# Kernel optimization log

Measured on AMD Instinct MI355X. Metric: run time of the kernel, lower is better.

Reference implementation:

```python
import jax, jax.numpy as jnp
import numpy as np
from jax import lax

V_, NC, SPW, H, B, T = 10000, 128, 64, 256, 16, 256  # C = NC*SPW = 8192
NEG = -1e9  # finite stand-in for -inf mask fill (grad-safe)


def _residual(x, w1, b1, w2, b2):
    # ResidualLayerOld: relu(lin2(relu(lin1(x)))) + x  (dropout=0 in eval)
    h = jax.nn.relu(x @ w1 + b1)
    return jax.nn.relu(h @ w2 + b2) + x


def _state_emb(e1, e2):
    # factored state embedding: state (c*SPW + j) -> e1[c] + e2[j]
    return (e1[:, None, :] + e2[None, :, :]).reshape(-1, e1.shape[-1])


def setup_inputs() -> dict:
    key = jax.random.key(0)
    ks = jax.random.split(key, 30)
    w2c = jax.random.randint(ks[0], (V_,), 0, NC)
    # brown-cluster style assignment: each word owns the SPW states of its cluster
    word2state = (w2c[:, None] * SPW + jnp.arange(SPW)[None, :]).astype(jnp.int32)
    text = jax.random.randint(ks[1], (B, T), 0, V_).astype(jnp.int32)

    def n(k, shape, s=0.05):
        return (jax.random.normal(k, shape) * s).astype(jnp.float32)

    z = lambda shape: jnp.zeros(shape, jnp.float32)
    return {
        "text": text, "word2state": word2state,
        "se1_start": n(ks[2], (NC, H), 1.0), "se2_start": n(ks[3], (SPW, H), 1.0),
        "start_w1": n(ks[4], (H, H)), "start_b1": z((H,)),
        "start_w2": n(ks[5], (H, H)), "start_b2": z((H,)),
        "start_pw": n(ks[6], (H, 1)), "start_pb": z((1,)),
        "se1_state": n(ks[7], (NC, H), 1.0), "se2_state": n(ks[8], (SPW, H), 1.0),
        "se1_next": n(ks[9], (NC, H), 1.0), "se2_next": n(ks[10], (SPW, H), 1.0),
        "trans_w1": n(ks[11], (H, H)), "trans_b1": z((H,)),
        "trans_w2": n(ks[12], (H, H)), "trans_b2": z((H,)),
        "se1_pre": n(ks[13], (NC, H), 1.0), "se2_pre": n(ks[14], (SPW, H), 1.0),
        "term_w1": n(ks[15], (H, H)), "term_b1": z((H,)),
        "term_w2": n(ks[16], (H, H)), "term_b2": z((H,)),
        "term_pw": n(ks[17], (H, V_)), "term_pb": z((V_,)),
    }


def reference(text, word2state,
              se1_start, se2_start, start_w1, start_b1, start_w2, start_b2,
              start_pw, start_pb,
              se1_state, se2_state, se1_next, se2_next,
              trans_w1, trans_b1, trans_w2, trans_b2,
              se1_pre, se2_pre, term_w1, term_b1, term_w2, term_b2,
              term_pw, term_pb):
    Vv, k = word2state.shape
    # start distribution over C states
    start_emb = _state_emb(se1_start, se2_start)                       # [C,H]
    start = jax.nn.log_softmax(
        (_residual(start_emb, start_w1, start_b1, start_w2, start_b2) @ start_pw
         + start_pb)[:, 0])                                            # [C]
    # transition: trans_mlp(state_emb) @ next_state_emb.T, row log_softmax
    state_emb = _state_emb(se1_state, se2_state)
    next_emb = _state_emb(se1_next, se2_next)
    transition = jax.nn.log_softmax(
        _residual(state_emb, trans_w1, trans_b1, trans_w2, trans_b2) @ next_emb.T,
        axis=-1)                                                       # [C,C]
    # emission: masked so state c only emits words whose word2state contains c
    pre_emb = _state_emb(se1_pre, se2_pre)
    C = pre_emb.shape[0]
    logits = _residual(pre_emb, term_w1, term_b1, term_w2, term_b2) @ term_pw + term_pb
    mask = jnp.zeros((C, Vv), dtype=bool).at[
        word2state.reshape(-1), jnp.repeat(jnp.arange(Vv), k)].set(True)
    emission = jax.nn.log_softmax(jnp.where(mask, logits, NEG), axis=-1)  # [C,V]
    # clamp to observed words
    cs = word2state[text]                                              # [B,T,k]
    pots = transition[cs[:, :-1, :, None], cs[:, 1:, None, :]]         # [B,T-1,k,k]
    obs = emission[cs, text[:, :, None]]                               # [B,T,k]
    alpha0 = start[cs[:, 0]] + obs[:, 0]                               # [B,k]

    def step(alpha, x):
        pot, o = x  # [B,k,k], [B,k]
        return jax.nn.logsumexp(alpha[:, :, None] + pot, axis=1) + o, None

    alpha, _ = lax.scan(step, alpha0,
                        (jnp.swapaxes(pots, 0, 1), jnp.swapaxes(obs[:, 1:], 0, 1)))
    return jax.nn.logsumexp(alpha, axis=-1)  # log p(text) per batch, [B]
```

## Files before the change

kernel.cpp:

```cpp
#include <hip/hip_runtime.h>
#include <hip/hip_bf16.h>
#include <math.h>

#define HH 256
#define NCC 128
#define SPWW 64
#define CST 8192
#define VV 10000
#define BBB 16
#define TTT 256
#define LOG2E 1.4426950408889634f
#define LN2 0.6931471805599453f

typedef __attribute__((ext_vector_type(8))) short short8;
typedef __attribute__((ext_vector_type(4))) float f32x4;
typedef unsigned short u16;

__device__ inline float bf2f(u16 u) {
    union { unsigned int i; float f; } v; v.i = ((unsigned int)u) << 16; return v.f;
}
__device__ inline u16 f2bf(float f) {
    __hip_bfloat16 h = __float2bfloat16(f);
    return *reinterpret_cast<u16*>(&h);
}
__device__ inline float ex2(float x) { return __builtin_amdgcn_exp2f(x); }
__device__ inline float lg2(float x) { return __builtin_amdgcn_logf(x); }

struct SetupA {
    const float* Ws[6]; u16* Wt;
    const float* pw; u16* pwT;
    const float* e1n; const float* e2n; u16* e1nb; u16* e2nb;
    const int* w2s; int* counts; int* offsets; int* wlist;
};
__global__ __launch_bounds__(256) void fhmm_setup(SetupA a)
{
    __shared__ float t[64][65];
    int blk = blockIdx.x, tid = threadIdx.x;
    if (blk < 96) {
        int z = blk >> 4, r = blk & 15;
        int k0 = (r & 3) * 64, n0 = (r >> 2) * 64;
        const float* W = a.Ws[z];
        u16* dst = a.Wt + (size_t)z * HH * HH;
        #pragma unroll
        for (int i = 0; i < 16; ++i) {
            int idx = tid + i * 256; int rr = idx >> 6, c = idx & 63;
            t[rr][c] = W[(k0 + rr) * HH + n0 + c];
        }
        __syncthreads();
        #pragma unroll
        for (int i = 0; i < 16; ++i) {
            int idx = tid + i * 256; int rr = idx >> 6, c = idx & 63;
            dst[(n0 + rr) * HH + k0 + c] = f2bf(t[c][rr]);
        }
    } else if (blk < 96 + 628) {
        int idx = blk - 96;
        int v0 = (idx % 157) * 64, k0 = (idx / 157) * 64;
        #pragma unroll
        for (int i = 0; i < 16; ++i) {
            int id2 = tid + i * 256; int rr = id2 >> 6, c = id2 & 63;
            int v = v0 + c;
            t[rr][c] = (v < VV) ? a.pw[(size_t)(k0 + rr) * VV + v] : 0.f;
        }
        __syncthreads();
        #pragma unroll
        for (int i = 0; i < 16; ++i) {
            int id2 = tid + i * 256; int rr = id2 >> 6, c = id2 & 63;
            int v = v0 + rr;
            if (v < VV) a.pwT[(size_t)v * HH + k0 + c] = f2bf(t[c][rr]);
        }
    } else if (blk < 96 + 628 + 128) {
        int idx = (blk - 724) * 256 + tid;
        if (idx < NCC * HH) a.e1nb[idx] = f2bf(a.e1n[idx]);
        if (idx < SPWW * HH) a.e2nb[idx] = f2bf(a.e2n[idx]);
    } else {
        __shared__ int cnt[NCC], off[NCC + 1], cur[NCC];
        if (tid < NCC) cnt[tid] = 0;
        __syncthreads();
        for (int v = tid; v < VV; v += 256)
            atomicAdd(&cnt[a.w2s[v * SPWW] >> 6], 1);
        __syncthreads();
        if (tid == 0) {
            int acc = 0;
            for (int c = 0; c < NCC; ++c) { off[c] = acc; acc += cnt[c]; }
            off[NCC] = acc;
        }
        __syncthreads();
        if (tid < NCC) cur[tid] = off[tid];
        __syncthreads();
        for (int v = tid; v < VV; v += 256) {
            int c = a.w2s[v * SPWW] >> 6;
            int pos = atomicAdd(&cur[c], 1);
            a.wlist[pos] = v;
        }
        if (tid < NCC) { a.counts[tid] = cnt[tid]; a.offsets[tid] = off[tid]; }
        if (tid == 0) a.offsets[NCC] = off[NCC];
    }
}

struct MlpA {
    const u16* X[3];
    const float* se1[3]; const float* se2[3];
    const u16* Wth[3];
    const float* bias[3];
    u16* Y[3];
    float oscale[3];
};
template<int LAYER>
__global__ __launch_bounds__(256) void fhmm_mlp_batch(MlpA a)
{
    int hd = blockIdx.z;
    int m0 = blockIdx.x * 64, n0 = blockIdx.y * 64;
    __shared__ char Xs[32768];
    __shared__ char Ws[32768];
    int tid = threadIdx.x, w = tid >> 6, lane = tid & 63, lr = lane & 15, lg = lane >> 4;
    const char* wsrc = (const char*)(a.Wth[hd] + (size_t)n0 * HH);
    if (LAYER == 0) {
        const float* s1 = a.se1[hd];
        const float* s2 = a.se2[hd];
        #pragma unroll
        for (int i = 0; i < 8; ++i) {
            int cc = i * 256 + tid; int row = cc >> 5, tt = cc & 31;
            int gm = m0 + row, k = tt * 8;
            const float* p1 = s1 + (gm >> 6) * HH + k;
            const float* p2 = s2 + (gm & 63) * HH + k;
            u16 pk[8];
            #pragma unroll
            for (int e = 0; e < 8; ++e) pk[e] = f2bf(p1[e] + p2[e]);
            int dst = row * 512 + ((tt ^ (row & 7)) << 4);
            *(uint4*)&Xs[dst] = *(uint4*)pk;
            *(uint4*)&Ws[dst] = *(const uint4*)(wsrc + cc * 16);
        }
    } else {
        const char* xsrc = (const char*)(a.X[hd] + (size_t)m0 * HH);
        #pragma unroll
        for (int i = 0; i < 8; ++i) {
            int cc = i * 256 + tid; int row = cc >> 5, tt = cc & 31;
            int dst = row * 512 + ((tt ^ (row & 7)) << 4);
            *(uint4*)&Xs[dst] = *(const uint4*)(xsrc + cc * 16);
            *(uint4*)&Ws[dst] = *(const uint4*)(wsrc + cc * 16);
        }
    }
    __syncthreads();
    short8 bfr[8];
    int brow = w * 16 + lr, bb = brow * 512, bsw = (brow & 7) << 4;
    #pragma unroll
    for (int ks = 0; ks < 8; ++ks)
        bfr[ks] = *(const short8*)(Ws + bb + (((ks * 4 + lg) << 4) ^ bsw));
    int cb = w * 16 + lg * 4;
    f32x4 bv = *(const f32x4*)(a.bias[hd] + n0 + cb);
    float osc = a.oscale[hd];
    u16* Yp = a.Y[hd];
    #pragma unroll
    for (int rm = 0; rm < 4; ++rm) {
        f32x4 acc = {0.f, 0.f, 0.f, 0.f};
        int ar = rm * 16 + lr, ab = ar * 512, asw = (ar & 7) << 4;
        #pragma unroll
        for (int ks = 0; ks < 8; ++ks) {
            short8 af = *(const short8*)(Xs + ab + (((ks * 4 + lg) << 4) ^ asw));
            acc = __builtin_amdgcn_mfma_f32_16x16x32_bf16(bfr[ks], af, acc, 0, 0, 0);
        }
        int gm = m0 + rm * 16 + lr;
        ushort4 o;
        if (LAYER == 1) {
            const float* r1 = a.se1[hd] + (gm >> 6) * HH + n0 + cb;
            const float* r2 = a.se2[hd] + (gm & 63) * HH + n0 + cb;
            #pragma unroll
            for (int e = 0; e < 4; ++e)
                ((u16*)&o)[e] = f2bf((fmaxf(acc[e] + bv[e], 0.f) + r1[e] + r2[e]) * osc);
        } else {
            #pragma unroll
            for (int e = 0; e < 4; ++e)
                ((u16*)&o)[e] = f2bf(fmaxf(acc[e] + bv[e], 0.f));
        }
        *(ushort4*)(Yp + (size_t)gm * HH + n0 + cb) = o;
    }
}

__global__ __launch_bounds__(256) void fhmm_gemm_uv(
    const u16* __restrict__ Abf, const u16* __restrict__ e1n,
    const u16* __restrict__ e2n, float* __restrict__ U2, float* __restrict__ V2)
{
    int y = blockIdx.y;
    int m0 = blockIdx.x * 64;
    const u16* Bb; float* C; int ldc;
    if (y < 2) { Bb = e1n + (size_t)y * 64 * HH; C = U2 + y * 64; ldc = NCC; }
    else       { Bb = e2n;                        C = V2;          ldc = SPWW; }
    __shared__ char Xs[32768];
    __shared__ char Ws[32768];
    int tid = threadIdx.x, w = tid >> 6, lane = tid & 63, lr = lane & 15, lg = lane >> 4;
    const char* xsrc = (const char*)(Abf + (size_t)m0 * HH);
    const char* wsrc = (const char*)Bb;
    #pragma unroll
    for (int i = 0; i < 8; ++i) {
        int cc = i * 256 + tid; int row = cc >> 5, tt = cc & 31;
        int dst = row * 512 + ((tt ^ (row & 7)) << 4);
        *(uint4*)&Xs[dst] = *(const uint4*)(xsrc + cc * 16);
        *(uint4*)&Ws[dst] = *(const uint4*)(wsrc + cc * 16);
    }
    __syncthreads();
    short8 bfr[8];
    int brow = w * 16 + lr, bb = brow * 512, bsw = (brow & 7) << 4;
    #pragma unroll
    for (int ks = 0; ks < 8; ++ks)
        bfr[ks] = *(const short8*)(Ws + bb + (((ks * 4 + lg) << 4) ^ bsw));
    int cb = w * 16 + lg * 4;
    #pragma unroll
    for (int rm = 0; rm < 4; ++rm) {
        f32x4 acc = {0.f, 0.f, 0.f, 0.f};
        int ar = rm * 16 + lr, ab = ar * 512, asw = (ar & 7) << 4;
        #pragma unroll
        for (int ks = 0; ks < 8; ++ks) {
            short8 af = *(const short8*)(Xs + ab + (((ks * 4 + lg) << 4) ^ asw));
            acc = __builtin_amdgcn_mfma_f32_16x16x32_bf16(bfr[ks], af, acc, 0, 0, 0);
        }
        int gm = m0 + rm * 16 + lr;
        *(f32x4*)(C + (size_t)gm * ldc + cb) = acc;
    }
}

__global__ __launch_bounds__(256) void fhmm_lse_uv(
    const float* __restrict__ U2, const float* __restrict__ V2,
    float* __restrict__ lse2)
{
    int tid = threadIdx.x, w = tid >> 6, lane = tid & 63;
    int s = blockIdx.x * 4 + w;
    float u0 = U2[(size_t)s * NCC + lane];
    float u1 = U2[(size_t)s * NCC + 64 + lane];
    float vv = V2[(size_t)s * SPWW + lane];
    float mu = fmaxf(u0, u1);
    #pragma unroll
    for (int d = 32; d; d >>= 1) mu = fmaxf(mu, __shfl_xor(mu, d));
    float su = ex2(u0 - mu) + ex2(u1 - mu);
    #pragma unroll
    for (int d = 32; d; d >>= 1) su += __shfl_xor(su, d);
    float mv = vv;
    #pragma unroll
    for (int d = 32; d; d >>= 1) mv = fmaxf(mv, __shfl_xor(mv, d));
    float sv = ex2(vv - mv);
    #pragma unroll
    for (int d = 32; d; d >>= 1) sv += __shfl_xor(sv, d);
    if (lane == 0) lse2[s] = (mu + lg2(su)) + (mv + lg2(sv));
}

__global__ __launch_bounds__(256) void fhmm_dotpw_kernel(
    const u16* __restrict__ hb, const float* __restrict__ pw,
    const float* __restrict__ pbp, float* __restrict__ p)
{
    int wv = threadIdx.x >> 6;
    int lane = threadIdx.x & 63;
    int s = blockIdx.x * 4 + wv;
    const u16* hr = hb + (size_t)s * HH;
    float acc = 0.f;
    #pragma unroll
    for (int i = 0; i < 4; ++i) acc += bf2f(hr[i * 64 + lane]) * pw[i * 64 + lane];
    #pragma unroll
    for (int d = 32; d; d >>= 1) acc += __shfl_xor(acc, d);
    if (lane == 0) p[s] = acc + pbp[0];
}

__global__ __launch_bounds__(1024) void fhmm_lsm_vec_kernel(float* __restrict__ p)
{
    __shared__ float red[64];
    int tid = threadIdx.x;
    float m = -1e30f;
    for (int i = tid; i < CST; i += 1024) m = fmaxf(m, p[i]);
    #pragma unroll
    for (int d = 32; d; d >>= 1) m = fmaxf(m, __shfl_xor(m, d));
    if ((tid & 63) == 0) red[tid >> 6] = m;
    __syncthreads();
    if (tid == 0) {
        float mm = red[0];
        for (int q = 1; q < 16; ++q) mm = fmaxf(mm, red[q]);
        red[32] = mm;
    }
    __syncthreads();
    float M = red[32];
    float s = 0.f;
    for (int i = tid; i < CST; i += 1024) s += expf(p[i] - M);
    #pragma unroll
    for (int d = 32; d; d >>= 1) s += __shfl_xor(s, d);
    if ((tid & 63) == 0) red[tid >> 6] = s;
    __syncthreads();
    if (tid == 0) {
        float ss = 0.f;
        for (int q = 0; q < 16; ++q) ss += red[q];
        red[33] = ss;
    }
    __syncthreads();
    float lse = M + logf(red[33]);
    for (int i = tid; i < CST; i += 1024) p[i] -= lse;
}

__global__ __launch_bounds__(256) void fhmm_ew_mfma(
    const u16* __restrict__ hpre_bf, const u16* __restrict__ pwT,
    const float* __restrict__ pb, const int* __restrict__ wlist,
    const int* __restrict__ counts, const int* __restrict__ offsets,
    float* __restrict__ Ew2, float* __restrict__ lse_em2)
{
    int c = blockIdx.x;
    int cnt = counts[c], off = offsets[c];
    __shared__ char Hs[32768];
    __shared__ float emM[4][64], emS[4][64];
    int tid = threadIdx.x, w = tid >> 6, lane = tid & 63, lr = lane & 15, lg = lane >> 4;
    const char* src = (const char*)(hpre_bf + (size_t)c * 64 * HH);
    #pragma unroll
    for (int i = 0; i < 8; ++i) {
        int cc = i * 256 + tid; int row = cc >> 5, tt = cc & 31;
        *(uint4*)&Hs[row * 512 + ((tt ^ (row & 7)) << 4)] = *(const uint4*)(src + cc * 16);
    }
    __syncthreads();

    float em_m[4][4], em_s[4][4];
    #pragma unroll
    for (int rm = 0; rm < 4; ++rm)
        #pragma unroll
        for (int e = 0; e < 4; ++e) { em_m[rm][e] = -3e38f; em_s[rm][e] = 0.f; }

    for (int ch = 0; ch * 64 < cnt; ++ch) {
        int widx = ch * 64 + w * 16 + lr;
        bool valid = widx < cnt;
        int v = valid ? wlist[off + widx] : 0;
        short8 bw[8];
        short8 bz = {0, 0, 0, 0, 0, 0, 0, 0};
        #pragma unroll
        for (int ks = 0; ks < 8; ++ks)
            bw[ks] = valid ? *(const short8*)(pwT + (size_t)v * HH + ks * 32 + lg * 8) : bz;
        float pbv = valid ? pb[v] : 0.f;
        #pragma unroll
        for (int rm = 0; rm < 4; ++rm) {
            f32x4 acc = {0.f, 0.f, 0.f, 0.f};
            int ar = rm * 16 + lr, ab = ar * 512, asw = (ar & 7) << 4;
            #pragma unroll
            for (int ks = 0; ks < 8; ++ks) {
                short8 ah = *(const short8*)(Hs + ab + (((ks * 4 + lg) << 4) ^ asw));
                acc = __builtin_amdgcn_mfma_f32_16x16x32_bf16(ah, bw[ks], acc, 0, 0, 0);
            }
            f32x4 o;
            #pragma unroll
            for (int e = 0; e < 4; ++e) o[e] = (acc[e] + pbv) * LOG2E;
            if (valid)
                *(f32x4*)(Ew2 + (size_t)v * 64 + rm * 16 + lg * 4) = o;
            #pragma unroll
            for (int e = 0; e < 4; ++e) {
                if (valid) {
                    float mn = fmaxf(em_m[rm][e], o[e]);
                    em_s[rm][e] = em_s[rm][e] * ex2(em_m[rm][e] - mn) + ex2(o[e] - mn);
                    em_m[rm][e] = mn;
                }
            }
        }
    }

    #pragma unroll
    for (int rm = 0; rm < 4; ++rm)
        #pragma unroll
        for (int e = 0; e < 4; ++e) {
            float mm = em_m[rm][e], ss = em_s[rm][e];
            #pragma unroll
            for (int d = 1; d < 16; d <<= 1) {
                float m2 = __shfl_xor(mm, d);
                float s2 = __shfl_xor(ss, d);
                float mn = fmaxf(mm, m2);
                ss = ss * ex2(mm - mn) + s2 * ex2(m2 - mn);
                mm = mn;
            }
            em_m[rm][e] = mm; em_s[rm][e] = ss;
        }
    if (lr == 0) {
        #pragma unroll
        for (int rm = 0; rm < 4; ++rm)
            #pragma unroll
            for (int e = 0; e < 4; ++e) {
                emM[w][rm * 16 + lg * 4 + e] = em_m[rm][e];
                emS[w][rm * 16 + lg * 4 + e] = em_s[rm][e];
            }
    }
    __syncthreads();
    if (tid < 64) {
        float M = emM[0][tid], S = emS[0][tid];
        #pragma unroll
        for (int q2 = 1; q2 < 4; ++q2) {
            float m2 = emM[q2][tid], s2 = emS[q2][tid];
            float mn = fmaxf(M, m2);
            S = S * ex2(M - mn) + s2 * ex2(m2 - mn); M = mn;
        }
        lse_em2[c * 64 + tid] = M + lg2(fmaxf(S, 1e-33f));
    }
}

template<int LEAF>
__global__ __launch_bounds__(256) void fhmm_combine4(
    const float* __restrict__ U2, const float* __restrict__ V2,
    const float* __restrict__ Ew2, const float* __restrict__ lse_em2,
    const float* __restrict__ lse2,
    const int* __restrict__ text, const int* __restrict__ w2s,
    const float* __restrict__ Lin, float* __restrict__ Lout)
{
    int p = blockIdx.x, b = blockIdx.y;
    int nodes = gridDim.x;
    int tid = threadIdx.x;
    int l6 = tid & 63, q = tid >> 6;

    __shared__ float Rb[64][65];
    __shared__ char Ps[8192], Qs[8192];
    __shared__ float mA2[64], mB2[64], mAf[64], mBf[64];
    __shared__ float part[2][4][64];
    __shared__ float rtB_l[64];

    int nm = LEAF ? ((p == 63) ? 3 : 4) : 4;
    int t0 = 4 * p + 1;
    int in0 = 4 * p;

    float va[16];
    float rowA = 0.f;

    if (LEAF) {
        int vprev = text[b * TTT + (t0 - 1)];
        int vA = text[b * TTT + t0];
        int srA = w2s[vprev * SPWW];
        int sA = w2s[vA * SPWW];
        int cA = sA >> 6;
        rowA = U2[(size_t)(srA + l6) * NCC + cA] - lse2[srA + l6];
        const float* vrow = V2 + (size_t)(srA + l6) * SPWW;
        const float* ewA = Ew2 + (size_t)vA * 64;
        const float* leA = lse_em2 + sA;
        #pragma unroll
        for (int jj = 0; jj < 16; ++jj) {
            int j = q * 16 + jj;
            va[jj] = vrow[j] + ewA[j] - leA[j];
        }
    } else {
        const float* Af = Lin + ((size_t)(b * (4 * nodes) + in0)) * 4096;
        #pragma unroll
        for (int jj = 0; jj < 16; ++jj)
            va[jj] = Af[l6 * 64 + q * 16 + jj];
    }

    for (int s = 1; s < nm; ++s) {
        float mloc = -3e38f;
        #pragma unroll
        for (int jj = 0; jj < 16; ++jj) mloc = fmaxf(mloc, va[jj]);
        part[0][q][l6] = mloc;

        float vb[16], obB = 0.f;
        if (LEAF) {
            int tB = t0 + s;
            int vBp = text[b * TTT + (tB - 1)];
            int vB = text[b * TTT + tB];
            int srB = w2s[vBp * SPWW];
            int sB = w2s[vB * SPWW];
            int cB = sB >> 6;
            if (tid < 64)
                rtB_l[tid] = U2[(size_t)(srB + tid) * NCC + cB] - lse2[srB + tid];
            obB = Ew2[(size_t)vB * 64 + l6] - lse_em2[sB + l6];
            float vraw[16];
            #pragma unroll
            for (int kk = 0; kk < 16; ++kk)
                vraw[kk] = V2[(size_t)(srB + q * 16 + kk) * SPWW + l6];
            __syncthreads();
            float mlocB = -3e38f;
            #pragma unroll
            for (int kk = 0; kk < 16; ++kk) {
                vb[kk] = vraw[kk] + rtB_l[q * 16 + kk];
                mlocB = fmaxf(mlocB, vb[kk]);
            }
            part[1][q][l6] = mlocB;
        } else {
            const float* Bf = Lin + ((size_t)(b * (4 * nodes) + in0 + s)) * 4096;
            float mlocB = -3e38f;
            #pragma unroll
            for (int kk = 0; kk < 16; ++kk) {
                float v = Bf[(q * 16 + kk) * 64 + l6];
                vb[kk] = v; mlocB = fmaxf(mlocB, v);
            }
            part[1][q][l6] = mlocB;
        }
        __syncthreads();

        if (tid < 64) {
            float mf = fmaxf(fmaxf(part[0][0][tid], part[0][1][tid]),
                             fmaxf(part[0][2][tid], part[0][3][tid]));
            mAf[tid] = mf;
            mA2[tid] = mf + ((LEAF && s == 1) ? rowA : 0.f);
        } else if (tid < 128) {
            int j = tid & 63;
            float mf = fmaxf(fmaxf(part[1][0][j], part[1][1][j]),
                             fmaxf(part[1][2][j], part[1][3][j]));
            mBf[j] = mf;
            mB2[j] = mf + obB;
        }
        __syncthreads();

        {
            float ma = mAf[l6];
            u16 pk[16];
            #pragma unroll
            for (int e = 0; e < 16; ++e) pk[e] = f2bf(ex2(va[e] - ma));
            uint4* srcv = (uint4*)pk;
            int base = l6 * 128;
            int s0 = 2 * q, s1 = 2 * q + 1, sw = (l6 & 7);
            *(uint4*)&Ps[base + ((s0 ^ sw) << 4)] = srcv[0];
            *(uint4*)&Ps[base + ((s1 ^ sw) << 4)] = srcv[1];
            float mb = mBf[l6];
            #pragma unroll
            for (int e = 0; e < 16; ++e) pk[e] = f2bf(ex2(vb[e] - mb));
            *(uint4*)&Qs[base + ((s0 ^ sw) << 4)] = srcv[0];
            *(uint4*)&Qs[base + ((s1 ^ sw) << 4)] = srcv[1];
        }
        __syncthreads();

        int w = q, lr = l6 & 15, lg = l6 >> 4;
        int brow = w * 16 + lr;
        short8 bfr[2];
        #pragma unroll
        for (int ks = 0; ks < 2; ++ks)
            bfr[ks] = *(const short8*)(Qs + brow * 128 + (((ks * 4 + lg) << 4) ^ ((brow & 7) << 4)));
        bool last = (s == nm - 1);
        float* Co = Lout + ((size_t)(b * nodes + p)) * 4096;
        #pragma unroll
        for (int rm = 0; rm < 4; ++rm) {
            f32x4 acc = {0.f, 0.f, 0.f, 0.f};
            int ar = rm * 16 + lr;
            #pragma unroll
            for (int ks = 0; ks < 2; ++ks) {
                short8 af = *(const short8*)(Ps + ar * 128 + (((ks * 4 + lg) << 4) ^ ((ar & 7) << 4)));
                acc = __builtin_amdgcn_mfma_f32_16x16x32_bf16(af, bfr[ks], acc, 0, 0, 0);
            }
            #pragma unroll
            for (int e = 0; e < 4; ++e) {
                int ii = rm * 16 + lg * 4 + e;
                int jj = w * 16 + lr;
                float cv = mA2[ii] + mB2[jj] + lg2(fmaxf(acc[e], 1e-33f));
                if (last) Co[ii * 64 + jj] = cv;
                else      Rb[ii][jj] = cv;
            }
        }
        if (!last) {
            __syncthreads();
            #pragma unroll
            for (int jj = 0; jj < 16; ++jj)
                va[jj] = Rb[l6][q * 16 + jj];
        }
    }
}

__global__ __launch_bounds__(256) void fhmm_tree_final(
    const float* __restrict__ Lin,
    const float* __restrict__ startv, const float* __restrict__ Ew2,
    const float* __restrict__ lse_em2,
    const int* __restrict__ text, const int* __restrict__ w2s,
    float* __restrict__ out)
{
    int b = blockIdx.x;
    int tid = threadIdx.x;
    int l6 = tid & 63, q = tid >> 6;

    __shared__ float Rb[64][65];
    __shared__ char Ps[8192], Qs[8192];
    __shared__ float mA2[64], mB2[64], mAf[64], mBf[64];
    __shared__ float part[2][4][64];
    __shared__ float a0[64];
    __shared__ float rm_[4], rs_[4];

    float va[16];
    {
        const float* Af = Lin + ((size_t)(b * 4)) * 4096;
        #pragma unroll
        for (int jj = 0; jj < 16; ++jj)
            va[jj] = Af[l6 * 64 + q * 16 + jj];
    }

    for (int s = 1; s < 4; ++s) {
        float mloc = -3e38f;
        #pragma unroll
        for (int jj = 0; jj < 16; ++jj) mloc = fmaxf(mloc, va[jj]);
        part[0][q][l6] = mloc;

        const float* Bf = Lin + ((size_t)(b * 4 + s)) * 4096;
        float vb[16];
        float mlocB = -3e38f;
        #pragma unroll
        for (int kk = 0; kk < 16; ++kk) {
            float v = Bf[(q * 16 + kk) * 64 + l6];
            vb[kk] = v; mlocB = fmaxf(mlocB, v);
        }
        part[1][q][l6] = mlocB;
        __syncthreads();

        if (tid < 64) {
            float mf = fmaxf(fmaxf(part[0][0][tid], part[0][1][tid]),
                             fmaxf(part[0][2][tid], part[0][3][tid]));
            mAf[tid] = mf; mA2[tid] = mf;
        } else if (tid < 128) {
            int j = tid & 63;
            float mf = fmaxf(fmaxf(part[1][0][j], part[1][1][j]),
                             fmaxf(part[1][2][j], part[1][3][j]));
            mBf[j] = mf; mB2[j] = mf;
        }
        __syncthreads();

        {
            float ma = mAf[l6];
            u16 pk[16];
            #pragma unroll
            for (int e = 0; e < 16; ++e) pk[e] = f2bf(ex2(va[e] - ma));
            uint4* srcv = (uint4*)pk;
            int base = l6 * 128;
            int s0 = 2 * q, s1 = 2 * q + 1, sw = (l6 & 7);
            *(uint4*)&Ps[base + ((s0 ^ sw) << 4)] = srcv[0];
            *(uint4*)&Ps[base + ((s1 ^ sw) << 4)] = srcv[1];
            float mb = mBf[l6];
            #pragma unroll
            for (int e = 0; e < 16; ++e) pk[e] = f2bf(ex2(vb[e] - mb));
            *(uint4*)&Qs[base + ((s0 ^ sw) << 4)] = srcv[0];
            *(uint4*)&Qs[base + ((s1 ^ sw) << 4)] = srcv[1];
        }
        __syncthreads();

        int w = q, lr = l6 & 15, lg = l6 >> 4;
        int brow = w * 16 + lr;
        short8 bfr[2];
        #pragma unroll
        for (int ks = 0; ks < 2; ++ks)
            bfr[ks] = *(const short8*)(Qs + brow * 128 + (((ks * 4 + lg) << 4) ^ ((brow & 7) << 4)));
        #pragma unroll
        for (int rm = 0; rm < 4; ++rm) {
            f32x4 acc = {0.f, 0.f, 0.f, 0.f};
            int ar = rm * 16 + lr;
            #pragma unroll
            for (int ks = 0; ks < 2; ++ks) {
                short8 af = *(const short8*)(Ps + ar * 128 + (((ks * 4 + lg) << 4) ^ ((ar & 7) << 4)));
                acc = __builtin_amdgcn_mfma_f32_16x16x32_bf16(af, bfr[ks], acc, 0, 0, 0);
            }
            #pragma unroll
            for (int e = 0; e < 4; ++e) {
                int ii = rm * 16 + lg * 4 + e;
                int jj = w * 16 + lr;
                Rb[ii][jj] = mA2[ii] + mB2[jj] + lg2(fmaxf(acc[e], 1e-33f));
            }
        }
        __syncthreads();
        if (s < 3) {
            #pragma unroll
            for (int jj = 0; jj < 16; ++jj)
                va[jj] = Rb[l6][q * 16 + jj];
        }
    }

    if (tid < 64) {
        int v0 = text[b * TTT];
        int s0 = w2s[v0 * SPWW];
        a0[tid] = startv[s0 + tid] * LOG2E + Ew2[(size_t)v0 * 64 + tid] - lse_em2[s0 + tid];
    }
    __syncthreads();
    float m = -3e38f, s = 0.f;
    for (int e = tid; e < 4096; e += 256) {
        float v = a0[e >> 6] + Rb[e >> 6][e & 63];
        float mn = fmaxf(m, v);
        s = s * ex2(m - mn) + ex2(v - mn);
        m = mn;
    }
    #pragma unroll
    for (int d = 32; d; d >>= 1) {
        float m2 = __shfl_xor(m, d), sx = __shfl_xor(s, d);
        float mn = fmaxf(m, m2);
        s = s * ex2(m - mn) + sx * ex2(m2 - mn); m = mn;
    }
    if ((tid & 63) == 0) { rm_[tid >> 6] = m; rs_[tid >> 6] = s; }
    __syncthreads();
    if (tid == 0) {
        float M_ = rm_[0], S_ = rs_[0];
        #pragma unroll
        for (int qq = 1; qq < 4; ++qq) {
            float mn = fmaxf(M_, rm_[qq]);
            S_ = S_ * ex2(M_ - mn) + rs_[qq] * ex2(rm_[qq] - mn); M_ = mn;
        }
        out[b] = (M_ + lg2(S_)) * LN2;
    }
}

extern "C" void kernel_launch(void* const* d_in, const int* in_sizes, int n_in,
                              void* d_out, int out_size, void* d_ws, size_t ws_size,
                              hipStream_t stream) {
    const int* text        = (const int*)d_in[0];
    const int* w2s         = (const int*)d_in[1];
    const float* se1_start = (const float*)d_in[2];
    const float* se2_start = (const float*)d_in[3];
    const float* start_w1  = (const float*)d_in[4];
    const float* start_b1  = (const float*)d_in[5];
    const float* start_w2  = (const float*)d_in[6];
    const float* start_b2  = (const float*)d_in[7];
    const float* start_pw  = (const float*)d_in[8];
    const float* start_pb  = (const float*)d_in[9];
    const float* se1_state = (const float*)d_in[10];
    const float* se2_state = (const float*)d_in[11];
    const float* se1_next  = (const float*)d_in[12];
    const float* se2_next  = (const float*)d_in[13];
    const float* trans_w1  = (const float*)d_in[14];
    const float* trans_b1  = (const float*)d_in[15];
    const float* trans_w2  = (const float*)d_in[16];
    const float* trans_b2  = (const float*)d_in[17];
    const float* se1_pre   = (const float*)d_in[18];
    const float* se2_pre   = (const float*)d_in[19];
    const float* term_w1   = (const float*)d_in[20];
    const float* term_b1   = (const float*)d_in[21];
    const float* term_w2   = (const float*)d_in[22];
    const float* term_b2   = (const float*)d_in[23];
    const float* term_pw   = (const float*)d_in[24];
    const float* term_pb   = (const float*)d_in[25];
    float* out = (float*)d_out;

    char* wp = (char*)d_ws;
    auto alloc = [&](size_t bytes) {
        char* p = wp;
        wp += (bytes + 255) & ~(size_t)255;
        return (void*)p;
    };
    u16* h1a         = (u16*)alloc((size_t)CST * HH * 2);
    u16* h1b         = (u16*)alloc((size_t)CST * HH * 2);
    u16* h1c         = (u16*)alloc((size_t)CST * HH * 2);
    u16* hstart_bf   = (u16*)alloc((size_t)CST * HH * 2);
    u16* h_state_bf  = (u16*)alloc((size_t)CST * HH * 2);
    u16* h_pre_bf    = (u16*)alloc((size_t)CST * HH * 2);
    u16* Wt          = (u16*)alloc((size_t)6 * HH * HH * 2);
    u16* pwT         = (u16*)alloc((size_t)VV * HH * 2);
    u16* e1n_bf      = (u16*)alloc((size_t)NCC * HH * 2);
    u16* e2n_bf      = (u16*)alloc((size_t)SPWW * HH * 2);
    float* U2        = (float*)alloc((size_t)CST * NCC * 4);
    float* V2        = (float*)alloc((size_t)CST * SPWW * 4);
    float* startv    = (float*)alloc(CST * 4);
    float* lse_trans = (float*)alloc(CST * 4);
    float* lse_em    = (float*)alloc(CST * 4);
    float* Ew        = (float*)alloc((size_t)VV * 64 * 4);
    int* counts      = (int*)alloc(NCC * 4);
    int* offsets     = (int*)alloc((NCC + 4) * 4);
    int* wlist       = (int*)alloc(VV * 4);
    float* LvA       = (float*)alloc((size_t)BBB * 64 * 4096 * 4);
    float* LvB       = (float*)alloc((size_t)BBB * 16 * 4096 * 4);
    float* LvC       = (float*)alloc((size_t)BBB * 4 * 4096 * 4);

    SetupA sa;
    sa.Ws[0] = start_w1; sa.Ws[1] = start_w2; sa.Ws[2] = trans_w1;
    sa.Ws[3] = trans_w2; sa.Ws[4] = term_w1;  sa.Ws[5] = term_w2;
    sa.Wt = Wt; sa.pw = term_pw; sa.pwT = pwT;
    sa.e1n = se1_next; sa.e2n = se2_next; sa.e1nb = e1n_bf; sa.e2nb = e2n_bf;
    sa.w2s = w2s; sa.counts = counts; sa.offsets = offsets; sa.wlist = wlist;
    hipLaunchKernelGGL(fhmm_setup, dim3(853), 256, 0, stream, sa);

    MlpA m1;
    m1.X[0] = m1.X[1] = m1.X[2] = nullptr;
    m1.se1[0] = se1_start; m1.se1[1] = se1_state; m1.se1[2] = se1_pre;
    m1.se2[0] = se2_start; m1.se2[1] = se2_state; m1.se2[2] = se2_pre;
    m1.Wth[0] = Wt + 0 * HH * HH; m1.Wth[1] = Wt + 2 * HH * HH; m1.Wth[2] = Wt + 4 * HH * HH;
    m1.bias[0] = start_b1; m1.bias[1] = trans_b1; m1.bias[2] = term_b1;
    m1.Y[0] = h1a; m1.Y[1] = h1b; m1.Y[2] = h1c;
    m1.oscale[0] = m1.oscale[1] = m1.oscale[2] = 1.0f;
    hipLaunchKernelGGL((fhmm_mlp_batch<0>), dim3(128, 4, 3), 256, 0, stream, m1);

    MlpA m2 = m1;
    m2.X[0] = h1a; m2.X[1] = h1b; m2.X[2] = h1c;
    m2.Wth[0] = Wt + 1 * HH * HH; m2.Wth[1] = Wt + 3 * HH * HH; m2.Wth[2] = Wt + 5 * HH * HH;
    m2.bias[0] = start_b2; m2.bias[1] = trans_b2; m2.bias[2] = term_b2;
    m2.Y[0] = hstart_bf; m2.Y[1] = h_state_bf; m2.Y[2] = h_pre_bf;
    m2.oscale[0] = 1.0f; m2.oscale[1] = LOG2E; m2.oscale[2] = 1.0f;
    hipLaunchKernelGGL((fhmm_mlp_batch<1>), dim3(128, 4, 3), 256, 0, stream, m2);

    hipLaunchKernelGGL(fhmm_dotpw_kernel, dim3(2048), 256, 0, stream,
                       hstart_bf, start_pw, start_pb, startv);
    hipLaunchKernelGGL(fhmm_lsm_vec_kernel, dim3(1), 1024, 0, stream, startv);

    hipLaunchKernelGGL(fhmm_gemm_uv, dim3(128, 3), 256, 0, stream,
                       h_state_bf, e1n_bf, e2n_bf, U2, V2);
    hipLaunchKernelGGL(fhmm_lse_uv, dim3(2048), 256, 0, stream, U2, V2, lse_trans);

    hipLaunchKernelGGL(fhmm_ew_mfma, dim3(NCC), 256, 0, stream,
                       h_pre_bf, pwT, term_pb, wlist, counts, offsets, Ew, lse_em);

    hipLaunchKernelGGL((fhmm_combine4<1>), dim3(64, BBB), 256, 0, stream,
                       U2, V2, Ew, lse_em, lse_trans, text, w2s,
                       (const float*)nullptr, LvA);
    hipLaunchKernelGGL((fhmm_combine4<0>), dim3(16, BBB), 256, 0, stream,
                       (const float*)nullptr, (const float*)nullptr,
                       (const float*)nullptr, (const float*)nullptr,
                       (const float*)nullptr, (const int*)nullptr,
                       (const int*)nullptr, LvA, LvB);
    hipLaunchKernelGGL((fhmm_combine4<0>), dim3(4, BBB), 256, 0, stream,
                       (const float*)nullptr, (const float*)nullptr,
                       (const float*)nullptr, (const float*)nullptr,
                       (const float*)nullptr, (const int*)nullptr,
                       (const int*)nullptr, LvB, LvC);

    hipLaunchKernelGGL(fhmm_tree_final, dim3(BBB), 256, 0, stream,
                       LvC, startv, Ew, lse_em, text, w2s, out);
}
```

Before: 125.6 us.

## Fuse start projection, UV log-sum-exp and start normalization into neighbouring kernels

The start head's final dot product with start_pw now runs in the second MLP layer's epilogue, using shuffles and atomicAdd into a zeroed startv buffer. This drops the separate dot kernel and the write of hstart_bf. The start log-softmax kernel is removed: its log-sum-exp is computed inside the combine kernel and subtracted from the final output, which is valid because start enters the likelihood once as an additive shift. The U/V GEMM and its row log-sum-exp are merged into one kernel that loops over the three weight tiles with online max/sum, trading 384 blocks for 128 and fewer launches and re-reads of U2/V2.

After: 126.5 us. Within noise of the previous version (+0.7%).

```diff
diff --git a/kernel.cpp b/kernel.cpp
--- a/kernel.cpp
+++ b/kernel.cpp
@@ -31,6 +31,7 @@
     const float* pw; u16* pwT;
     const float* e1n; const float* e2n; u16* e1nb; u16* e2nb;
     const int* w2s; int* counts; int* offsets; int* wlist;
+    float* startv;
 };
 __global__ __launch_bounds__(256) void fhmm_setup(SetupA a)
 {
@@ -52,7 +53,7 @@
             int idx = tid + i * 256; int rr = idx >> 6, c = idx & 63;
             dst[(n0 + rr) * HH + k0 + c] = f2bf(t[c][rr]);
         }
-    } else if (blk < 96 + 628) {
+    } else if (blk < 724) {
         int idx = blk - 96;
         int v0 = (idx % 157) * 64, k0 = (idx / 157) * 64;
         #pragma unroll
@@ -68,10 +69,13 @@
             int v = v0 + rr;
             if (v < VV) a.pwT[(size_t)v * HH + k0 + c] = f2bf(t[c][rr]);
         }
-    } else if (blk < 96 + 628 + 128) {
+    } else if (blk < 852) {
         int idx = (blk - 724) * 256 + tid;
         if (idx < NCC * HH) a.e1nb[idx] = f2bf(a.e1n[idx]);
         if (idx < SPWW * HH) a.e2nb[idx] = f2bf(a.e2n[idx]);
+    } else if (blk < 884) {
+        int idx = (blk - 852) * 256 + tid;
+        if (idx < CST) a.startv[idx] = 0.f;
     } else {
         __shared__ int cnt[NCC], off[NCC + 1], cur[NCC];
         if (tid < NCC) cnt[tid] = 0;
@@ -104,6 +108,8 @@
     const float* bias[3];
     u16* Y[3];
     float oscale[3];
+    const float* pw;
+    float* startv;
 };
 template<int LAYER>
 __global__ __launch_bounds__(256) void fhmm_mlp_batch(MlpA a)
@@ -160,135 +166,139 @@
             acc = __builtin_amdgcn_mfma_f32_16x16x32_bf16(bfr[ks], af, acc, 0, 0, 0);
         }
         int gm = m0 + rm * 16 + lr;
-        ushort4 o;
         if (LAYER == 1) {
             const float* r1 = a.se1[hd] + (gm >> 6) * HH + n0 + cb;
             const float* r2 = a.se2[hd] + (gm & 63) * HH + n0 + cb;
+            float vals[4];
             #pragma unroll
             for (int e = 0; e < 4; ++e)
-                ((u16*)&o)[e] = f2bf((fmaxf(acc[e] + bv[e], 0.f) + r1[e] + r2[e]) * osc);
+                vals[e] = fmaxf(acc[e] + bv[e], 0.f) + r1[e] + r2[e];
+            if (hd == 0) {
+                const float* pwc = a.pw + n0 + cb;
+                float dotp = vals[0] * pwc[0] + vals[1] * pwc[1]
+                           + vals[2] * pwc[2] + vals[3] * pwc[3];
+                dotp += __shfl_xor(dotp, 16);
+                dotp += __shfl_xor(dotp, 32);
+                if (lg == 0) atomicAdd(&a.startv[gm], dotp);
+            } else {
+                ushort4 o;
+                #pragma unroll
+                for (int e = 0; e < 4; ++e) ((u16*)&o)[e] = f2bf(vals[e] * osc);
+                *(ushort4*)(Yp + (size_t)gm * HH + n0 + cb) = o;
+            }
         } else {
+            ushort4 o;
             #pragma unroll
             for (int e = 0; e < 4; ++e)
                 ((u16*)&o)[e] = f2bf(fmaxf(acc[e] + bv[e], 0.f));
-        }
-        *(ushort4*)(Yp + (size_t)gm * HH + n0 + cb) = o;
+            *(ushort4*)(Yp + (size_t)gm * HH + n0 + cb) = o;
+        }
     }
 }
 
-__global__ __launch_bounds__(256) void fhmm_gemm_uv(
+__global__ __launch_bounds__(256) void fhmm_gemm_uv_lse(
     const u16* __restrict__ Abf, const u16* __restrict__ e1n,
-    const u16* __restrict__ e2n, float* __restrict__ U2, float* __restrict__ V2)
+    const u16* __restrict__ e2n, float* __restrict__ U2, float* __restrict__ V2,
+    float* __restrict__ lse_trans2)
 {
-    int y = blockIdx.y;
     int m0 = blockIdx.x * 64;
-    const u16* Bb; float* C; int ldc;
-    if (y < 2) { Bb = e1n + (size_t)y * 64 * HH; C = U2 + y * 64; ldc = NCC; }
-    else       { Bb = e2n;                        C = V2;          ldc = SPWW; }
     __shared__ char Xs[32768];
     __shared__ char Ws[32768];
+    __shared__ float lmU[4][64], lsU[4][64], lmV[4][64], lsV[4][64];
     int tid = threadIdx.x, w = tid >> 6, lane = tid & 63, lr = lane & 15, lg = lane >> 4;
     const char* xsrc = (const char*)(Abf + (size_t)m0 * HH);
-    const char* wsrc = (const char*)Bb;
     #pragma unroll
     for (int i = 0; i < 8; ++i) {
         int cc = i * 256 + tid; int row = cc >> 5, tt = cc & 31;
         int dst = row * 512 + ((tt ^ (row & 7)) << 4);
         *(uint4*)&Xs[dst] = *(const uint4*)(xsrc + cc * 16);
-        *(uint4*)&Ws[dst] = *(const uint4*)(wsrc + cc * 16);
-    }
-    __syncthreads();
-    short8 bfr[8];
-    int brow = w * 16 + lr, bb = brow * 512, bsw = (brow & 7) << 4;
+    }
+
+    float mU[4], sU[4], mV[4], sV[4];
     #pragma unroll
-    for (int ks = 0; ks < 8; ++ks)
-        bfr[ks] = *(const short8*)(Ws + bb + (((ks * 4 + lg) << 4) ^ bsw));
+    for (int rm = 0; rm < 4; ++rm) { mU[rm] = -3e38f; sU[rm] = 0.f; mV[rm] = -3e38f; sV[rm] = 0.f; }
+
     int cb = w * 16 + lg * 4;
+    for (int y = 0; y < 3; ++y) {
+        const char* wsrc = (y < 2) ? (const char*)(e1n + (size_t)y * 64 * HH)
+                                   : (const char*)e2n;
+        __syncthreads();
+        #pragma unroll
+        for (int i = 0; i < 8; ++i) {
+            int cc = i * 256 + tid; int row = cc >> 5, tt = cc & 31;
+            int dst = row * 512 + ((tt ^ (row & 7)) << 4);
+            *(uint4*)&Ws[dst] = *(const uint4*)(wsrc + cc * 16);
+        }
+        __syncthreads();
+        short8 bfr[8];
+        int brow = w * 16 + lr, bb = brow * 512, bsw = (brow & 7) << 4;
+        #pragma unroll
+        for (int ks = 0; ks < 8; ++ks)
+            bfr[ks] = *(const short8*)(Ws + bb + (((ks * 4 + lg) << 4) ^ bsw));
+        #pragma unroll
+        for (int rm = 0; rm < 4; ++rm) {
+            f32x4 acc = {0.f, 0.f, 0.f, 0.f};
+            int ar = rm * 16 + lr, ab = ar * 512, asw = (ar & 7) << 4;
+            #pragma unroll
+            for (int ks = 0; ks < 8; ++ks) {
+                short8 af = *(const short8*)(Xs + ab + (((ks * 4 + lg) << 4) ^ asw));
+                acc = __builtin_amdgcn_mfma_f32_16x16x32_bf16(bfr[ks], af, acc, 0, 0, 0);
+            }
+            int gm = m0 + rm * 16 + lr;
+            float lm = fmaxf(fmaxf(acc[0], acc[1]), fmaxf(acc[2], acc[3]));
+            if (y < 2) {
+                *(f32x4*)(U2 + (size_t)gm * NCC + y * 64 + cb) = acc;
+                float mn = fmaxf(mU[rm], lm);
+                sU[rm] = sU[rm] * ex2(mU[rm] - mn)
+                       + ex2(acc[0] - mn) + ex2(acc[1] - mn)
+                       + ex2(acc[2] - mn) + ex2(acc[3] - mn);
+                mU[rm] = mn;
+            } else {
+                *(f32x4*)(V2 + (size_t)gm * SPWW + cb) = acc;
+                float mn = fmaxf(mV[rm], lm);
+                sV[rm] = sV[rm] * ex2(mV[rm] - mn)
+                       + ex2(acc[0] - mn) + ex2(acc[1] - mn)
+                       + ex2(acc[2] - mn) + ex2(acc[3] - mn);
+                mV[rm] = mn;
+            }
+        }
+    }
+
     #pragma unroll
     for (int rm = 0; rm < 4; ++rm) {
-        f32x4 acc = {0.f, 0.f, 0.f, 0.f};
-        int ar = rm * 16 + lr, ab = ar * 512, asw = (ar & 7) << 4;
-        #pragma unroll
-        for (int ks = 0; ks < 8; ++ks) {
-            short8 af = *(const short8*)(Xs + ab + (((ks * 4 + lg) << 4) ^ asw));
-            acc = __builtin_amdgcn_mfma_f32_16x16x32_bf16(bfr[ks], af, acc, 0, 0, 0);
-        }
-        int gm = m0 + rm * 16 + lr;
-        *(f32x4*)(C + (size_t)gm * ldc + cb) = acc;
-    }
-}
-
-__global__ __launch_bounds__(256) void fhmm_lse_uv(
-    const float* __restrict__ U2, const float* __restrict__ V2,
-    float* __restrict__ lse2)
-{
-    int tid = threadIdx.x, w = tid >> 6, lane = tid & 63;
-    int s = blockIdx.x * 4 + w;
-    float u0 = U2[(size_t)s * NCC + lane];
-    float u1 = U2[(size_t)s * NCC + 64 + lane];
-    float vv = V2[(size_t)s * SPWW + lane];
-    float mu = fmaxf(u0, u1);
-    #pragma unroll
-    for (int d = 32; d; d >>= 1) mu = fmaxf(mu, __shfl_xor(mu, d));
-    float su = ex2(u0 - mu) + ex2(u1 - mu);
-    #pragma unroll
-    for (int d = 32; d; d >>= 1) su += __shfl_xor(su, d);
-    float mv = vv;
-    #pragma unroll
-    for (int d = 32; d; d >>= 1) mv = fmaxf(mv, __shfl_xor(mv, d));
-    float sv = ex2(vv - mv);
-    #pragma unroll
-    for (int d = 32; d; d >>= 1) sv += __shfl_xor(sv, d);
-    if (lane == 0) lse2[s] = (mu + lg2(su)) + (mv + lg2(sv));
-}
-
-__global__ __launch_bounds__(256) void fhmm_dotpw_kernel(
-    const u16* __restrict__ hb, const float* __restrict__ pw,
-    const float* __restrict__ pbp, float* __restrict__ p)
-{
-    int wv = threadIdx.x >> 6;
-    int lane = threadIdx.x & 63;
-    int s = blockIdx.x * 4 + wv;
-    const u16* hr = hb + (size_t)s * HH;
-    float acc = 0.f;
-    #pragma unroll
-    for (int i = 0; i < 4; ++i) acc += bf2f(hr[i * 64 + lane]) * pw[i * 64 + lane];
-    #pragma unroll
-    for (int d = 32; d; d >>= 1) acc += __shfl_xor(acc, d);
-    if (lane == 0) p[s] = acc + pbp[0];
-}
-
-__global__ __launch_bounds__(1024) void fhmm_lsm_vec_kernel(float* __restrict__ p)
-{
-    __shared__ float red[64];
-    int tid = threadIdx.x;
-    float m = -1e30f;
-    for (int i = tid; i < CST; i += 1024) m = fmaxf(m, p[i]);
-    #pragma unroll
-    for (int d = 32; d; d >>= 1) m = fmaxf(m, __shfl_xor(m, d));
-    if ((tid & 63) == 0) red[tid >> 6] = m;
+        #pragma unroll
+        for (int d = 16; d < 64; d <<= 1) {
+            float m2 = __shfl_xor(mU[rm], d), sx = __shfl_xor(sU[rm], d);
+            float mn = fmaxf(mU[rm], m2);
+            sU[rm] = sU[rm] * ex2(mU[rm] - mn) + sx * ex2(m2 - mn); mU[rm] = mn;
+            m2 = __shfl_xor(mV[rm], d); sx = __shfl_xor(sV[rm], d);
+            mn = fmaxf(mV[rm], m2);
+            sV[rm] = sV[rm] * ex2(mV[rm] - mn) + sx * ex2(m2 - mn); mV[rm] = mn;
+        }
+    }
     __syncthreads();
-    if (tid == 0) {
-        float mm = red[0];
-        for (int q = 1; q < 16; ++q) mm = fmaxf(mm, red[q]);
-        red[32] = mm;
+    if (lg == 0) {
+        #pragma unroll
+        for (int rm = 0; rm < 4; ++rm) {
+            lmU[w][rm * 16 + lr] = mU[rm]; lsU[w][rm * 16 + lr] = sU[rm];
+            lmV[w][rm * 16 + lr] = mV[rm]; lsV[w][rm * 16 + lr] = sV[rm];
+        }
     }
     __syncthreads();
-    float M = red[32];
-    float s = 0.f;
-    for (int i = tid; i < CST; i += 1024) s += expf(p[i] - M);
-    #pragma unroll
-    for (int d = 32; d; d >>= 1) s += __shfl_xor(s, d);
-    if ((tid & 63) == 0) red[tid >> 6] = s;
-    __syncthreads();
-    if (tid == 0) {
-        float ss = 0.f;
-        for (int q = 0; q < 16; ++q) ss += red[q];
-        red[33] = ss;
-    }
-    __syncthreads();
-    float lse = M + logf(red[33]);
-    for (int i = tid; i < CST; i += 1024) p[i] -= lse;
+    if (tid < 64) {
+        float MU = lmU[0][tid], SU = lsU[0][tid];
+        float MV = lmV[0][tid], SV = lsV[0][tid];
+        #pragma unroll
+        for (int q = 1; q < 4; ++q) {
+            float m2 = lmU[q][tid], sx = lsU[q][tid];
+            float mn = fmaxf(MU, m2);
+            SU = SU * ex2(MU - mn) + sx * ex2(m2 - mn); MU = mn;
+            m2 = lmV[q][tid]; sx = lsV[q][tid];
+            mn = fmaxf(MV, m2);
+            SV = SV * ex2(MV - mn) + sx * ex2(m2 - mn); MV = mn;
+        }
+        lse_trans2[m0 + tid] = (MU + lg2(SU)) + (MV + lg2(SV));
+    }
 }
 
 __global__ __launch_bounds__(256) void fhmm_ew_mfma(
@@ -561,6 +571,35 @@
     __shared__ float part[2][4][64];
     __shared__ float a0[64];
     __shared__ float rm_[4], rs_[4];
+    __shared__ float lse_start_s;
+
+    {
+        float m = -3e38f, s = 0.f;
+        for (int i = tid; i < CST; i += 256) {
+            float v = startv[i] * LOG2E;
+            float mn = fmaxf(m, v);
+            s = s * ex2(m - mn) + ex2(v - mn);
+            m = mn;
+        }
+        #pragma unroll
+        for (int d = 32; d; d >>= 1) {
+            float m2 = __shfl_xor(m, d), sx = __shfl_xor(s, d);
+            float mn = fmaxf(m, m2);
+            s = s * ex2(m - mn) + sx * ex2(m2 - mn); m = mn;
+        }
+        if ((tid & 63) == 0) { rm_[tid >> 6] = m; rs_[tid >> 6] = s; }
+        __syncthreads();
+        if (tid == 0) {
+            float M_ = rm_[0], S_ = rs_[0];
+            #pragma unroll
+            for (int qq = 1; qq < 4; ++qq) {
+                float mn = fmaxf(M_, rm_[qq]);
+                S_ = S_ * ex2(M_ - mn) + rs_[qq] * ex2(rm_[qq] - mn); M_ = mn;
+            }
+            lse_start_s = M_ + lg2(S_);
+        }
+        __syncthreads();
+    }
 
     float va[16];
     {
@@ -675,7 +714,7 @@
             float mn = fmaxf(M_, rm_[qq]);
             S_ = S_ * ex2(M_ - mn) + rs_[qq] * ex2(rm_[qq] - mn); M_ = mn;
         }
-        out[b] = (M_ + lg2(S_)) * LN2;
+        out[b] = (M_ + lg2(S_) - lse_start_s) * LN2;
     }
 }
 
@@ -719,7 +758,6 @@
     u16* h1a         = (u16*)alloc((size_t)CST * HH * 2);
     u16* h1b         = (u16*)alloc((size_t)CST * HH * 2);
     u16* h1c         = (u16*)alloc((size_t)CST * HH * 2);
-    u16* hstart_bf   = (u16*)alloc((size_t)CST * HH * 2);
     u16* h_state_bf  = (u16*)alloc((size_t)CST * HH * 2);
     u16* h_pre_bf    = (u16*)alloc((size_t)CST * HH * 2);
     u16* Wt          = (u16*)alloc((size_t)6 * HH * HH * 2);
@@ -738,6 +776,7 @@
     float* LvA       = (float*)alloc((size_t)BBB * 64 * 4096 * 4);
     float* LvB       = (float*)alloc((size_t)BBB * 16 * 4096 * 4);
     float* LvC       = (float*)alloc((size_t)BBB * 4 * 4096 * 4);
+    u16* dummyY      = (u16*)alloc(256 * 2);
 
     SetupA sa;
     sa.Ws[0] = start_w1; sa.Ws[1] = start_w2; sa.Ws[2] = trans_w1;
@@ -745,7 +784,8 @@
     sa.Wt = Wt; sa.pw = term_pw; sa.pwT = pwT;
     sa.e1n = se1_next; sa.e2n = se2_next; sa.e1nb = e1n_bf; sa.e2nb = e2n_bf;
     sa.w2s = w2s; sa.counts = counts; sa.offsets = offsets; sa.wlist = wlist;
-    hipLaunchKernelGGL(fhmm_setup, dim3(853), 256, 0, stream, sa);
+    sa.startv = startv;
+    hipLaunchKernelGGL(fhmm_setup, dim3(885), 256, 0, stream, sa);
 
     MlpA m1;
     m1.X[0] = m1.X[1] = m1.X[2] = nullptr;
@@ -755,23 +795,19 @@
     m1.bias[0] = start_b1; m1.bias[1] = trans_b1; m1.bias[2] = term_b1;
     m1.Y[0] = h1a; m1.Y[1] = h1b; m1.Y[2] = h1c;
     m1.oscale[0] = m1.oscale[1] = m1.oscale[2] = 1.0f;
+    m1.pw = start_pw; m1.startv = startv;
     hipLaunchKernelGGL((fhmm_mlp_batch<0>), dim3(128, 4, 3), 256, 0, stream, m1);
 
     MlpA m2 = m1;
     m2.X[0] = h1a; m2.X[1] = h1b; m2.X[2] = h1c;
     m2.Wth[0] = Wt + 1 * HH * HH; m2.Wth[1] = Wt + 3 * HH * HH; m2.Wth[2] = Wt + 5 * HH * HH;
     m2.bias[0] = start_b2; m2.bias[1] = trans_b2; m2.bias[2] = term_b2;
-    m2.Y[0] = hstart_bf; m2.Y[1] = h_state_bf; m2.Y[2] = h_pre_bf;
+    m2.Y[0] = dummyY; m2.Y[1] = h_state_bf; m2.Y[2] = h_pre_bf;
     m2.oscale[0] = 1.0f; m2.oscale[1] = LOG2E; m2.oscale[2] = 1.0f;
     hipLaunchKernelGGL((fhmm_mlp_batch<1>), dim3(128, 4, 3), 256, 0, stream, m2);
 
-    hipLaunchKernelGGL(fhmm_dotpw_kernel, dim3(2048), 256, 0, stream,
-                       hstart_bf, start_pw, start_pb, startv);
-    hipLaunchKernelGGL(fhmm_lsm_vec_kernel, dim3(1), 1024, 0, stream, startv);
-
-    hipLaunchKernelGGL(fhmm_gemm_uv, dim3(128, 3), 256, 0, stream,
-                       h_state_bf, e1n_bf, e2n_bf, U2, V2);
-    hipLaunchKernelGGL(fhmm_lse_uv, dim3(2048), 256, 0, stream, U2, V2, lse_trans);
+    hipLaunchKernelGGL(fhmm_gemm_uv_lse, dim3(128), 256, 0, stream,
+                       h_state_bf, e1n_bf, e2n_bf, U2, V2, lse_trans);
 
     hipLaunchKernelGGL(fhmm_ew_mfma, dim3(NCC), 256, 0, stream,
                        h_pre_bf, pwT, term_pb, wlist, counts, offsets, Ew, lse_em);
```
